# Performance work log

Measured on AMD Instinct MI355X. Metric: run time of the kernel, lower is better.

The kernel has to match this reference:

```python
import jax, jax.numpy as jnp
import numpy as np

N_RNA, N_DIS = 40000, 3000
E_EDGES, T = 600000, 10000
RNA_IN, D_FEAT, HID, EXP_D = 512, 256, 512, 256
N_EXP, HEADS = 8, 8
HD = HID // HEADS          # per-head dim inside HANConv
MHA_HD = EXP_D // HEADS    # per-head dim in cross-attention
FUSION = 2 * HID


def setup_inputs() -> dict:
    key = jax.random.key(0)
    ks = iter(jax.random.split(key, 48))
    def nrm(shape, s=0.02):
        return jax.random.normal(next(ks), shape, dtype=jnp.float32) * s
    inp = {
        "x_rna": jax.random.normal(next(ks), (N_RNA, RNA_IN), dtype=jnp.float32),
        "x_dis": jax.random.normal(next(ks), (N_DIS, D_FEAT), dtype=jnp.float32),
        "Wd": nrm((RNA_IN, D_FEAT)), "bd": jnp.zeros((RNA_IN,), jnp.float32),
        "Wp_r": nrm((HID, RNA_IN)), "bp_r": jnp.zeros((HID,), jnp.float32),
        "Wp_d": nrm((HID, RNA_IN)), "bp_d": jnp.zeros((HID,), jnp.float32),
        "a_src_rd": nrm((HEADS, HD), 0.1), "a_dst_rd": nrm((HEADS, HD), 0.1),
        "a_src_dr": nrm((HEADS, HD), 0.1), "a_dst_dr": nrm((HEADS, HD), 0.1),
        "kW": nrm((HID, HID)), "kb": jnp.zeros((HID,), jnp.float32),
        "qv": nrm((HID,), 0.1),
        "Wl": nrm((HID, HID)), "bl": jnp.zeros((HID,), jnp.float32),
        "W_exp": nrm((N_EXP, FUSION, EXP_D)), "b_exp": jnp.zeros((N_EXP, EXP_D), jnp.float32),
        "W_gate": nrm((4, HID, N_EXP)),
        "W_head": nrm((4, 2 * EXP_D, EXP_D)), "b_head": jnp.zeros((4, EXP_D), jnp.float32),
        "in_w": nrm((3 * EXP_D, EXP_D)), "in_b": jnp.zeros((3 * EXP_D,), jnp.float32),
        "out_w": nrm((EXP_D, EXP_D)), "out_b": jnp.zeros((EXP_D,), jnp.float32),
        "Wdp": nrm((EXP_D, HID)), "bdp": jnp.zeros((EXP_D,), jnp.float32),
        "ei_rd_src": jax.random.randint(next(ks), (E_EDGES,), 0, N_RNA),
        "ei_rd_dst": jax.random.randint(next(ks), (E_EDGES,), 0, N_DIS),
        "ei_dr_src": jax.random.randint(next(ks), (E_EDGES,), 0, N_DIS),
        "ei_dr_dst": jax.random.randint(next(ks), (E_EDGES,), 0, N_RNA),
        "idx_rels": jax.random.randint(next(ks), (4, T), 0, N_RNA),
    }
    return inp


def _han_edge(x_src, x_dst, ei_src, ei_dst, a_src, a_dst, n_dst):
    # x_*: [N, H, D]; GAT-style attention with softmax per destination node (PyG HANConv edge step)
    as_ = (x_src * a_src).sum(-1)                                 # [Ns, H]
    ad_ = (x_dst * a_dst).sum(-1)                                 # [Nd, H]
    alpha = jax.nn.leaky_relu(as_[ei_src] + ad_[ei_dst], 0.2)     # [E, H]
    amax = jax.ops.segment_max(alpha, ei_dst, num_segments=n_dst)
    ex = jnp.exp(alpha - amax[ei_dst])
    den = jax.ops.segment_sum(ex, ei_dst, num_segments=n_dst)
    w = ex / (den[ei_dst] + 1e-16)
    msg = x_src[ei_src] * w[:, :, None]                           # [E, H, D]
    out = jax.ops.segment_sum(msg, ei_dst, num_segments=n_dst)    # [Nd, H, D]
    return jax.nn.relu(out.reshape(n_dst, -1))


def _semantic(outs, kW, kb, qv):
    # outs: [M, N, F]; metapath-level (semantic) attention from HANConv
    s = (jnp.tanh(outs @ kW.T + kb).mean(axis=1) * qv).sum(-1)    # [M]
    beta = jax.nn.softmax(s)
    return (beta[:, None, None] * outs).sum(0)


def reference(x_rna, x_dis, Wd, bd, Wp_r, bp_r, Wp_d, bp_d,
              a_src_rd, a_dst_rd, a_src_dr, a_dst_dr,
              kW, kb, qv, Wl, bl, W_exp, b_exp, W_gate, W_head, b_head,
              in_w, in_b, out_w, out_b, Wdp, bdp,
              ei_rd_src, ei_rd_dst, ei_dr_src, ei_dr_dst, idx_rels):
    # ---- HAN encoder ----
    xd = x_dis @ Wd.T + bd                                        # disease feat -> rna_in_dim
    hr0 = (x_rna @ Wp_r.T + bp_r).reshape(N_RNA, HEADS, HD)
    hd0 = (xd @ Wp_d.T + bp_d).reshape(N_DIS, HEADS, HD)
    out_dis = _han_edge(hr0, hd0, ei_rd_src, ei_rd_dst, a_src_rd, a_dst_rd, N_DIS)
    out_rna = _han_edge(hd0, hr0, ei_dr_src, ei_dr_dst, a_src_dr, a_dst_dr, N_RNA)
    h_rna = _semantic(out_rna[None], kW, kb, qv) @ Wl.T + bl      # shared final lin
    h_dis = _semantic(out_dis[None], kW, kb, qv) @ Wl.T + bl
    # ---- MoE with per-relation gating ----
    d_global = h_dis.mean(axis=0)
    fusion = jnp.concatenate([h_rna, jnp.broadcast_to(d_global, h_rna.shape)], axis=1)  # [N, 2H]
    E = jax.nn.relu(jnp.einsum('nf,efd->ned', fusion, W_exp) + b_exp)  # [N, Nexp, Ed]
    h_t = h_rna[idx_rels]                                         # [4, T, H]
    scores = jnp.einsum('rth,rhe->rte', h_t, W_gate)              # raw gate scores (no softmax)
    u = (E[idx_rels] * scores[..., None]).sum(axis=2)             # [4, T, Ed]
    U = u.mean(axis=1)                                            # [4, Ed]
    # ---- cross attention over 4 task tokens ----
    qkv = U @ in_w.T + in_b
    q, k, v = jnp.split(qkv, 3, axis=-1)
    def heads(z):
        return z.reshape(4, HEADS, MHA_HD).transpose(1, 0, 2)     # [H, 4, dh]
    qh, kh, vh = heads(q), heads(k), heads(v)
    attn = jax.nn.softmax(jnp.einsum('htd,hsd->hts', qh, kh) / np.float32(np.sqrt(MHA_HD)), axis=-1)
    o = jnp.einsum('hts,hsd->htd', attn, vh).transpose(1, 0, 2).reshape(4, EXP_D)
    U_prime = o @ out_w.T + out_b                                 # [4, Ed]
    # ---- per-relation heads and disease scores ----
    cross = jnp.broadcast_to(U_prime[:, None, :], u.shape)
    cat = jnp.concatenate([u, cross], axis=-1)                    # [4, T, 2Ed]
    p = jax.nn.relu(jnp.einsum('rtc,rcd->rtd', cat, W_head) + b_head[:, None, :])
    d_proj = h_dis @ Wdp.T + bdp                                  # [Ndis, Ed]
    return jax.nn.sigmoid(jnp.einsum('rtd,md->rtm', p, d_proj))   # [4, T, Ndis]
```

## Files before the change

kernel.cpp:

```cpp
#include <hip/hip_runtime.h>
#include <math.h>

constexpr int NRNA = 40000;
constexpr int NDIS = 3000;
constexpr int NEDG = 600000;
constexpr int TREL = 10000;

typedef __attribute__((ext_vector_type(8))) short bh8;
typedef __attribute__((ext_vector_type(4))) float f32x4;

__device__ inline float bf2f(ushort x) {
    union { uint u; float f; } v; v.u = ((uint)x) << 16; return v.f;
}
__device__ inline ushort f2bf(float f) {
    union { float f; uint u; } v; v.f = f;
    uint u = v.u;
    uint r = (u + 0x7fffu + ((u >> 16) & 1u)) >> 16;
    return (ushort)r;
}
__device__ inline float bflo(uint w) { union { uint u; float f; } v; v.u = w << 16; return v.f; }
__device__ inline float bfhi(uint w) { union { uint u; float f; } v; v.u = w & 0xffff0000u; return v.f; }

__device__ inline void gload16(const ushort* g, ushort* l) {
    __builtin_amdgcn_global_load_lds(
        (const __attribute__((address_space(1))) unsigned int*)(const void*)g,
        (__attribute__((address_space(3))) unsigned int*)(void*)l, 16, 0, 0);
}

__global__ __launch_bounds__(256) void conv_bf16(const float* __restrict__ in,
                                                 ushort* __restrict__ out, long n)
{
    long g = ((long)blockIdx.x * 256 + threadIdx.x) * 4;
    if (g >= n) return;
    float4 v = *(const float4*)(in + g);
    ushort4 o;
    o.x = f2bf(v.x); o.y = f2bf(v.y); o.z = f2bf(v.z); o.w = f2bf(v.w);
    *(ushort4*)(out + g) = o;
}

__global__ __launch_bounds__(256) void transpose_wexp(const float* __restrict__ W,
                                                      ushort* __restrict__ out)
{
    long g = (long)blockIdx.x * 256 + threadIdx.x;
    int e = (int)(g >> 17), d = (int)((g >> 9) & 255), f = (int)(g & 511);
    out[g] = f2bf(W[(long)e * 262144 + (long)f * 256 + d]);
}

__global__ __launch_bounds__(256) void transpose_whead(const float* __restrict__ W,
                                                       ushort* __restrict__ out)
{
    long g = (long)blockIdx.x * 256 + threadIdx.x;
    int r = (int)(g >> 16), d = (int)((g >> 8) & 255), c = (int)(g & 255);
    out[g] = f2bf(W[(long)r * 131072 + (long)c * 256 + d]);
}

__global__ void transpose_wgate(const float* __restrict__ W, float* __restrict__ out)
{
    int g = blockIdx.x * 256 + threadIdx.x;
    int r = g >> 12, e = (g >> 9) & 7, k = g & 511;
    out[g] = W[(long)r * 4096 + (long)k * 8 + e];
}

template<int ACT>
__global__ __launch_bounds__(256) void gemm_mfma(
    const ushort* __restrict__ A, const ushort* __restrict__ B,
    const float* __restrict__ bias, float* __restrict__ Cf, ushort* __restrict__ Cb,
    const int* __restrict__ idx,
    int M, int N, int K, long sA, long sB, long sBias, long sC)
{
    __shared__ ushort smem[16384];
    ushort* As = smem;
    ushort* Bs = smem + 8192;
    const int bz = blockIdx.z;
    const ushort* Ab = A + (long)bz * sA;
    const ushort* Bb = B + (long)bz * sB;
    const float* biasb = bias ? (bias + (long)bz * sBias) : nullptr;
    const int row0 = blockIdx.y * 128, col0 = blockIdx.x * 128;

    const int tid = threadIdx.x, wid = tid >> 6, lane = tid & 63;
    const int wr = wid >> 1, wc = wid & 1;

    const int lrow = lane >> 3;
    const int lk = (((lane & 7) ^ lrow) * 8);
    const ushort* ap0[4]; const ushort* bp0[4];
    ushort* la[4]; ushort* lb[4];
#pragma unroll
    for (int i = 0; i < 4; ++i) {
        int c = wid * 4 + i;
        int ra = row0 + c * 8 + lrow; ra = ra < M ? ra : M - 1;
        int rs = idx ? idx[ra] : ra;
        ap0[i] = Ab + (long)rs * K + lk;
        int cb = col0 + c * 8 + lrow; cb = cb < N ? cb : N - 1;
        bp0[i] = Bb + (long)cb * K + lk;
        la[i] = As + c * 512;
        lb[i] = Bs + c * 512;
    }

    f32x4 acc[4][4];
#pragma unroll
    for (int i = 0; i < 4; ++i)
#pragma unroll
        for (int n = 0; n < 4; ++n) acc[i][n] = (f32x4){0.f, 0.f, 0.f, 0.f};

    const int fr = lane & 15, fq = lane >> 4;
    const int sw0 = (fq ^ (fr & 7)) * 8;
    const ushort* paRow = As + (wr * 64 + fr) * 64;
    const ushort* pbRow = Bs + (wc * 64 + fr) * 64;

    for (int k0 = 0; k0 < K; k0 += 64) {
#pragma unroll
// ... 37 lines not shown
            int cl = (tid & 15) * 4;
            int m = row0 + rl, col = col0 + H * 64 + cl;
            if (m < M && col < N) {
                f32x4 v = *(const f32x4*)(cs + rl * 64 + cl);
                if (biasb) {
                    float4 bv = *(const float4*)(biasb + col);
                    v[0] += bv.x; v[1] += bv.y; v[2] += bv.z; v[3] += bv.w;
                }
                if (ACT == 1) {
#pragma unroll
                    for (int q = 0; q < 4; ++q) v[q] = fmaxf(v[q], 0.f);
                } else if (ACT == 2) {
#pragma unroll
                    for (int q = 0; q < 4; ++q) v[q] = 1.f / (1.f + __expf(-v[q]));
                }
                long o = (long)bz * sC + (long)m * N + col;
                if (Cf) *(f32x4*)(Cf + o) = v;
                if (Cb) {
                    ushort4 ob;
                    ob.x = f2bf(v[0]); ob.y = f2bf(v[1]); ob.z = f2bf(v[2]); ob.w = f2bf(v[3]);
                    *(ushort4*)(Cb + o) = ob;
                }
            }
        }
        __syncthreads();
    }
}

__global__ __launch_bounds__(256) void moe_mfma(
    const ushort* __restrict__ h, const ushort* __restrict__ WexpT,
    const float* __restrict__ c_exp, const float* __restrict__ S,
    const int* __restrict__ idx, ushort* __restrict__ up)
{
    __shared__ ushort smem[16384];
    __shared__ float sS[128 * 8];
    __shared__ float sC[8 * 128];
    ushort* As = smem;
    ushort* Bs = smem + 8192;
    const int row0 = blockIdx.y * 128, col0 = blockIdx.x * 128;
    const int z = blockIdx.z, e0 = z * 4;
    const int tid = threadIdx.x, wid = tid >> 6, lane = tid & 63;
    const int wr = wid >> 1, wc = wid & 1;
    constexpr int M = 4 * TREL;

    for (int i = tid; i < 1024; i += 256) {
        int rr = i >> 3, e = i & 7;
        sS[i] = S[(long)(row0 + rr) * 8 + e];
        int ee = i >> 7, cc = i & 127;
        sC[i] = c_exp[ee * 256 + col0 + cc];
    }

    const int lrow = lane >> 3;
    const int lk = (((lane & 7) ^ lrow) * 8);
    const ushort* ap0[4]; const ushort* bp0[4];
    ushort* la[4]; ushort* lb[4];
#pragma unroll
    for (int i = 0; i < 4; ++i) {
        int c = wid * 4 + i;
        int ra = row0 + c * 8 + lrow;
        ap0[i] = h + (long)idx[ra] * 512 + lk;
        bp0[i] = WexpT + (long)(col0 + c * 8 + lrow) * 512 + (long)e0 * 131072 + lk;
        la[i] = As + c * 512;
        lb[i] = Bs + c * 512;
    }

    const int fr = lane & 15, fq = lane >> 4;
    const int sw0 = (fq ^ (fr & 7)) * 8;
    const ushort* paRow = As + (wr * 64 + fr) * 64;
    const ushort* pbRow = Bs + (wc * 64 + fr) * 64;

    f32x4 uacc[4][4];
#pragma unroll
    for (int i = 0; i < 4; ++i)
#pragma unroll
        for (int n = 0; n < 4; ++n) uacc[i][n] = (f32x4){0.f, 0.f, 0.f, 0.f};
    __syncthreads();

    for (int el = 0; el < 4; ++el) {
        const int e = e0 + el;
        f32x4 acc[4][4];
#pragma unroll
        for (int i = 0; i < 4; ++i)
#pragma unroll
            for (int n = 0; n < 4; ++n) acc[i][n] = (f32x4){0.f, 0.f, 0.f, 0.f};
        const long boff = (long)el * 131072;
        for (int k0 = 0; k0 < 512; k0 += 64) {
#pragma unroll
            for (int i = 0; i < 4; ++i) gload16(ap0[i] + k0, la[i]);
#pragma unroll
            for (int i = 0; i < 4; ++i) gload16(bp0[i] + boff + k0, lb[i]);
            __syncthreads();
#pragma unroll
            for (int kk = 0; kk < 2; ++kk) {
                const int sw = kk ? (sw0 ^ 32) : sw0;
                bh8 af[4], bf[4];
#pragma unroll
                for (int i = 0; i < 4; ++i) af[i] = *(const bh8*)(paRow + i * 1024 + sw);
#pragma unroll
                for (int n = 0; n < 4; ++n) bf[n] = *(const bh8*)(pbRow + n * 1024 + sw);
#pragma unroll
                for (int i = 0; i < 4; ++i)
#pragma unroll
                    for (int n = 0; n < 4; ++n)
                        acc[i][n] = __builtin_amdgcn_mfma_f32_16x16x32_bf16(af[i], bf[n], acc[i][n], 0, 0, 0);
            }
            __syncthreads();
        }
#pragma unroll
        for (int i = 0; i < 4; ++i) {
            int rl = wr * 64 + i * 16 + fq * 4;
#pragma unroll
            for (int n = 0; n < 4; ++n) {
                int cl = wc * 64 + n * 16 + fr;
                float c = sC[e * 128 + cl];
#pragma unroll
                for (int r = 0; r < 4; ++r) {
                    float s = sS[(rl + r) * 8 + e];
                    float v = acc[i][n][r] + c;
                    uacc[i][n][r] = fmaf(s, fmaxf(v, 0.f), uacc[i][n][r]);
                }
            }
        }
    }

    float* cs = (float*)smem;
    ushort* upz = up + (long)z * M * 256;
#pragma unroll
    for (int H = 0; H < 2; ++H) {
        if (wc == H) {
#pragma unroll
            for (int i = 0; i < 4; ++i)
#pragma unroll
                for (int n = 0; n < 4; ++n)
#pragma unroll
                    for (int r = 0; r < 4; ++r)
                        cs[(wr * 64 + i * 16 + fq * 4 + r) * 64 + n * 16 + fr] = uacc[i][n][r];
        }
        __syncthreads();
#pragma unroll
        for (int it = 0; it < 8; ++it) {
            int rl = it * 16 + (tid >> 4);
            int cl = (tid & 15) * 4;
            f32x4 v = *(const f32x4*)(cs + rl * 64 + cl);
            int m = row0 + rl, col = col0 + H * 64 + cl;
            ushort4 ob;
            ob.x = f2bf(v[0]); ob.y = f2bf(v[1]); ob.z = f2bf(v[2]); ob.w = f2bf(v[3]);
            *(ushort4*)(upz + (long)m * 256 + col) = ob;
        }
        __syncthreads();
    }
}

__global__ __launch_bounds__(256) void moe_combine(const ushort* __restrict__ up,
                                                   ushort* __restrict__ u)
{
    constexpr long TOT = (long)4 * TREL * 256;
    long g = ((long)blockIdx.x * 256 + threadIdx.x) * 4;
    if (g >= TOT) return;
    ushort4 a = *(const ushort4*)(up + g);
    ushort4 b = *(const ushort4*)(up + TOT + g);
    ushort4 o;
    o.x = f2bf(bf2f(a.x) + bf2f(b.x));
    o.y = f2bf(bf2f(a.y) + bf2f(b.y));
    o.z = f2bf(bf2f(a.z) + bf2f(b.z));
    o.w = f2bf(bf2f(a.w) + bf2f(b.w));
    *(ushort4*)(u + g) = o;
}

__global__ void dot_heads_bf(const ushort* __restrict__ x, const float* __restrict__ a,
                             float* __restrict__ out, int nodes)
{
    long g = (long)blockIdx.x * 256 + threadIdx.x;
    if (g >= (long)nodes * 8) return;
    int node = (int)(g >> 3), h = (int)(g & 7);
    const ushort* xp = x + (long)node * 512 + h * 64;
    const float* ap = a + h * 64;
    float s = 0.f;
#pragma unroll
    for (int d = 0; d < 64; d += 8) {
        uint4 xv = *(const uint4*)(xp + d);
        float4 a0 = *(const float4*)(ap + d);
        float4 a1 = *(const float4*)(ap + d + 4);
        s += bflo(xv.x) * a0.x + bfhi(xv.x) * a0.y + bflo(xv.y) * a0.z + bfhi(xv.y) * a0.w;
        s += bflo(xv.z) * a1.x + bfhi(xv.z) * a1.y + bflo(xv.w) * a1.z + bfhi(xv.w) * a1.w;
    }
    out[g] = s;
}

__global__ void hist_kernel(const int* __restrict__ dst, int* __restrict__ deg, int E)
{
    int g = blockIdx.x * 256 + threadIdx.x;
    if (g < E) atomicAdd(&deg[dst[g]], 1);
}

__global__ __launch_bounds__(1024) void scan_blocks(const int* __restrict__ in,
                                                    int* __restrict__ tmp,
                                                    int* __restrict__ bsum, int n)
{
    __shared__ int wsum[16];
    const int tid = threadIdx.x, lane = tid & 63, wid = tid >> 6;
    int base = blockIdx.x * 1024;
    int v = (base + tid < n) ? in[base + tid] : 0;
    int s = v;
#pragma unroll
    for (int off = 1; off < 64; off <<= 1) {
        int t = __shfl_up(s, off, 64);
        if (lane >= off) s += t;
    }
    if (lane == 63) wsum[wid] = s;
    __syncthreads();
    if (wid == 0) {
        int w = (lane < 16) ? wsum[lane] : 0;
#pragma unroll
        for (int off = 1; off < 16; off <<= 1) {
            int t = __shfl_up(w, off, 64);
            if (lane >= off) w += t;
        }
        if (lane < 16) wsum[lane] = w;
    }
// ... 12 lines not shown
        int t = __shfl_up(v, off, 64);
        if (lane >= off) v += t;
    }
    if (lane < nb) bsum[lane] = v;
}

__global__ __launch_bounds__(1024) void scan_finish(const int* __restrict__ in,
                                                    const int* __restrict__ tmp,
                                                    const int* __restrict__ bsum,
                                                    int* __restrict__ offs,
                                                    int* __restrict__ cur, int n, int nb)
{
    int base = blockIdx.x * 1024;
    int i = base + threadIdx.x;
    if (i < n) {
        int pre = (blockIdx.x == 0) ? 0 : bsum[blockIdx.x - 1];
        int v = tmp[i] - in[i] + pre;
        offs[i] = v;
        cur[i] = v;
    }
    if (i == 0) offs[n] = bsum[nb - 1];
}

__global__ void scatter_kernel(const int* __restrict__ src, const int* __restrict__ dst,
                               int* __restrict__ cur, int* __restrict__ csr_src, int E)
{
    int g = blockIdx.x * 256 + threadIdx.x;
    if (g < E) {
        int p = atomicAdd(&cur[dst[g]], 1);
        csr_src[p] = src[g];
    }
}

__global__ __launch_bounds__(256) void han_aggregate(
    const int* __restrict__ offs, const int* __restrict__ csr_src,
    const float* __restrict__ as_, const float* __restrict__ ad_,
    const ushort* __restrict__ x_src, ushort* __restrict__ out)
{
    const int node = blockIdx.x;
    const int tid = threadIdx.x;
    const int e0 = offs[node], e1 = offs[node + 1];
    const int ne = e1 - e0;

    __shared__ float s_amax[8], s_den[8];
    __shared__ float s_ex[32 * 8];
    __shared__ int   s_srcs[32];
    __shared__ float s_red[256];
    __shared__ float s_part[4 * 512];

    const int myh = tid & 7;
    const float my_ad = ad_[node * 8 + myh];

    float mx = -3.0e38f;
    for (int i = tid; i < ne * 8; i += 256) {
        int src = csr_src[e0 + (i >> 3)];
        float al = as_[(long)src * 8 + myh] + my_ad;
        al = al >= 0.f ? al : 0.2f * al;
        mx = fmaxf(mx, al);
    }
    s_red[tid] = mx;
    __syncthreads();
    if (tid < 8) {
        float m = -3.0e38f;
        for (int j = tid; j < 256; j += 8) m = fmaxf(m, s_red[j]);
        s_amax[tid] = m;
    }
    __syncthreads();
    const float myamax = s_amax[myh];

    const int g = tid >> 6, l64 = tid & 63, col8 = l64 * 8, gh = l64 >> 3;
    float acc[8];
#pragma unroll
    for (int k = 0; k < 8; ++k) acc[k] = 0.f;
    float dpart = 0.f;

    for (int c0 = 0; c0 < ne; c0 += 32) {
        const int nc = min(32, ne - c0);
        __syncthreads();
        if (tid < nc * 8) {
            int ec = tid >> 3;
            int src = csr_src[e0 + c0 + ec];
            if (myh == 0) s_srcs[ec] = src;
            float al = as_[(long)src * 8 + myh] + my_ad;
            al = al >= 0.f ? al : 0.2f * al;
            float ex = __expf(al - myamax);
            s_ex[ec * 8 + myh] = ex;
            dpart += ex;
        }
        __syncthreads();
        for (int j2 = 0; j2 < 8; ++j2) {
            int jj = j2 * 4 + g;
            if (jj >= nc) break;
            float w = s_ex[jj * 8 + gh];
            uint4 xv = *(const uint4*)(x_src + (long)s_srcs[jj] * 512 + col8);
            acc[0] = fmaf(w, bflo(xv.x), acc[0]);
            acc[1] = fmaf(w, bfhi(xv.x), acc[1]);
            acc[2] = fmaf(w, bflo(xv.y), acc[2]);
            acc[3] = fmaf(w, bfhi(xv.y), acc[3]);
            acc[4] = fmaf(w, bflo(xv.z), acc[4]);
            acc[5] = fmaf(w, bfhi(xv.z), acc[5]);
            acc[6] = fmaf(w, bflo(xv.w), acc[6]);
            acc[7] = fmaf(w, bfhi(xv.w), acc[7]);
        }
    }

    s_red[tid] = dpart;
    __syncthreads();
    if (tid < 8) {
        float s = 0.f;
        for (int j = tid; j < 256; j += 8) s += s_red[j];
        s_den[tid] = s;
    }
#pragma unroll
    for (int k = 0; k < 8; ++k) s_part[g * 512 + col8 + k] = acc[k];
    __syncthreads();

    int c2 = tid * 2;
    float v0 = s_part[c2] + s_part[512 + c2] + s_part[1024 + c2] + s_part[1536 + c2];
    float v1 = s_part[c2 + 1] + s_part[512 + c2 + 1] + s_part[1024 + c2 + 1] + s_part[1536 + c2 + 1];
    float den = s_den[c2 >> 6] + 1e-16f;
    ushort2 o;
    o.x = f2bf(fmaxf(v0 / den, 0.f));
    o.y = f2bf(fmaxf(v1 / den, 0.f));
    *(ushort2*)(out + (long)node * 512 + c2) = o;
}

__global__ __launch_bounds__(512) void hdis_colsum_partial(const float* __restrict__ h_dis,
                                                           float* __restrict__ part)
{
    int c = blockIdx.x, d = threadIdx.x;
    int r0 = c * 200;
    float s = 0.f;
    for (int r = r0; r < r0 + 200; ++r) s += h_dis[(long)r * 512 + d];
    part[c * 512 + d] = s;
}
__global__ __launch_bounds__(512) void hdis_colsum_finish(const float* __restrict__ part,
                                                          float* __restrict__ dg)
{
    int d = threadIdx.x;
    float s = 0.f;
    for (int c = 0; c < 15; ++c) s += part[c * 512 + d];
    dg[d] = s * (1.f / NDIS);
}

__global__ void cexp_kernel(const float* __restrict__ dg, const float* __restrict__ W_exp,
                            const float* __restrict__ b_exp, float* __restrict__ c_exp)
{
    int e = blockIdx.x, d = threadIdx.x;
    const float* W = W_exp + (long)e * 1024 * 256 + 512 * 256 + d;
    float s = b_exp[e * 256 + d];
    for (int f = 0; f < 512; ++f) s = fmaf(dg[f], W[(long)f * 256], s);
    c_exp[e * 256 + d] = s;
}

__global__ __launch_bounds__(256) void scores2(const ushort* __restrict__ h,
                                               const float* __restrict__ WgT,
                                               const int* __restrict__ idx,
                                               float* __restrict__ S)
{
    __shared__ float sW[8 * 512];
    const int r = blockIdx.y;
    const int tid = threadIdx.x;
    for (int i = tid; i < 4096; i += 256) sW[i] = WgT[(long)r * 4096 + i];
    __syncthreads();
    int n = blockIdx.x * 256 + tid;
    if (n >= TREL) return;
    int gi = r * TREL + n;
    const ushort* hp = h + (long)idx[gi] * 512;
    float acc[8];
#pragma unroll
    for (int e = 0; e < 8; ++e) acc[e] = 0.f;
    for (int k = 0; k < 512; k += 8) {
        uint4 hv = *(const uint4*)(hp + k);
        float hf[8];
        hf[0] = bflo(hv.x); hf[1] = bfhi(hv.x); hf[2] = bflo(hv.y); hf[3] = bfhi(hv.y);
        hf[4] = bflo(hv.z); hf[5] = bfhi(hv.z); hf[6] = bflo(hv.w); hf[7] = bfhi(hv.w);
#pragma unroll
        for (int e = 0; e < 8; ++e)
#pragma unroll
            for (int j = 0; j < 8; ++j)
                acc[e] = fmaf(hf[j], sW[e * 512 + k + j], acc[e]);
    }
#pragma unroll
    for (int e = 0; e < 8; ++e) S[(long)gi * 8 + e] = acc[e];
// ... 102 lines not shown
    const float* a_dst_dr = (const float*)d_in[11];
    const float* Wl       = (const float*)d_in[15];
    const float* bl       = (const float*)d_in[16];
    const float* W_exp    = (const float*)d_in[17];
    const float* b_exp    = (const float*)d_in[18];
    const float* W_gate   = (const float*)d_in[19];
    const float* W_head   = (const float*)d_in[20];
    const float* b_head   = (const float*)d_in[21];
    const float* in_w     = (const float*)d_in[22];
    const float* in_b     = (const float*)d_in[23];
    const float* out_w    = (const float*)d_in[24];
    const float* out_b    = (const float*)d_in[25];
    const float* Wdp      = (const float*)d_in[26];
    const float* bdp      = (const float*)d_in[27];
    const int* ei_rd_src  = (const int*)d_in[28];
    const int* ei_rd_dst  = (const int*)d_in[29];
    const int* ei_dr_src  = (const int*)d_in[30];
    const int* ei_dr_dst  = (const int*)d_in[31];
    const int* idx_rels   = (const int*)d_in[32];
    float* out = (float*)d_out;

    char* ws = (char*)d_ws;
    size_t off = 0;
    auto alloc = [&](size_t bytes) -> void* {
        off = (off + 255) & ~(size_t)255;
        void* p = ws + off;
        off += bytes;
        return p;
    };
    ushort* xrb      = (ushort*)alloc((size_t)NRNA * 512 * 2);
    ushort* hr0b     = (ushort*)alloc((size_t)NRNA * 512 * 2);
    ushort* u_bf     = (ushort*)alloc((size_t)4 * TREL * 256 * 2);
    ushort* p_bf     = (ushort*)alloc((size_t)4 * TREL * 256 * 2);
    ushort* up_bf    = (ushort*)alloc((size_t)2 * 4 * TREL * 256 * 2);
    ushort* xdb      = (ushort*)alloc((size_t)NDIS * 256 * 2);
    ushort* xd_bf    = (ushort*)alloc((size_t)NDIS * 512 * 2);
    ushort* hd0b     = (ushort*)alloc((size_t)NDIS * 512 * 2);
    ushort* outdis_b = (ushort*)alloc((size_t)NDIS * 512 * 2);
    ushort* hdis_b   = (ushort*)alloc((size_t)NDIS * 512 * 2);
    ushort* dproj_b  = (ushort*)alloc((size_t)NDIS * 256 * 2);
    float*  hdis_f   = (float*)alloc((size_t)NDIS * 512 * 4);
    ushort* Wdb    = (ushort*)alloc((size_t)512 * 256 * 2);
    ushort* Wprb   = (ushort*)alloc((size_t)512 * 512 * 2);
    ushort* Wpdb   = (ushort*)alloc((size_t)512 * 512 * 2);
    ushort* Wlb    = (ushort*)alloc((size_t)512 * 512 * 2);
    ushort* Wdpb   = (ushort*)alloc((size_t)256 * 512 * 2);
    ushort* WexpT  = (ushort*)alloc((size_t)8 * 256 * 512 * 2);
    ushort* WheadT = (ushort*)alloc((size_t)4 * 256 * 256 * 2);
    float*  WgT    = (float*)alloc((size_t)4 * 8 * 512 * 4);
    float* as_rd   = (float*)alloc((size_t)NRNA * 8 * 4);
    float* ad_rd   = (float*)alloc((size_t)NDIS * 8 * 4);
    float* as_dr   = (float*)alloc((size_t)NDIS * 8 * 4);
    float* ad_dr   = (float*)alloc((size_t)NRNA * 8 * 4);
    float* S       = (float*)alloc((size_t)4 * TREL * 8 * 4);
    float* dg_part = (float*)alloc((size_t)15 * 512 * 4);
    float* dg      = (float*)alloc((size_t)512 * 4);
    float* c_exp   = (float*)alloc((size_t)8 * 256 * 4);
    float* u_part  = (float*)alloc((size_t)4 * 32 * 256 * 4);
    float* U       = (float*)alloc((size_t)4 * 256 * 4);
    float* Up      = (float*)alloc((size_t)4 * 256 * 4);
    float* c_head  = (float*)alloc((size_t)4 * 256 * 4);
    int* deg_rd  = (int*)alloc((size_t)NDIS * 4);
    int* offs_rd = (int*)alloc((size_t)(NDIS + 1) * 4);
    int* cur_rd  = (int*)alloc((size_t)NDIS * 4);
    int* csr_rd  = (int*)alloc((size_t)NEDG * 4);
    int* deg_dr  = (int*)alloc((size_t)NRNA * 4);
    int* offs_dr = (int*)alloc((size_t)(NRNA + 1) * 4);
    int* cur_dr  = (int*)alloc((size_t)NRNA * 4);
    int* csr_dr  = (int*)alloc((size_t)NEDG * 4);
    int* scan_tmp = (int*)alloc((size_t)NRNA * 4);
    int* scan_bs  = (int*)alloc((size_t)64 * 4);
    if (off > ws_size) return;

    ushort* outrna_b = xrb;
    ushort* hrna_b   = hr0b;

    const dim3 blk(256);

    conv_bf16<<<dim3(20000), blk, 0, stream>>>(x_rna, xrb, (long)NRNA * 512);
    conv_bf16<<<dim3(750),   blk, 0, stream>>>(x_dis, xdb, (long)NDIS * 256);
    conv_bf16<<<dim3(128),   blk, 0, stream>>>(Wd,   Wdb,  512 * 256);
    conv_bf16<<<dim3(256),   blk, 0, stream>>>(Wp_r, Wprb, 512 * 512);
    conv_bf16<<<dim3(256),   blk, 0, stream>>>(Wp_d, Wpdb, 512 * 512);
    conv_bf16<<<dim3(256),   blk, 0, stream>>>(Wl,   Wlb,  512 * 512);
    conv_bf16<<<dim3(128),   blk, 0, stream>>>(Wdp,  Wdpb, 256 * 512);
    transpose_wexp<<<dim3(4096), blk, 0, stream>>>(W_exp, WexpT);
    transpose_whead<<<dim3(1024), blk, 0, stream>>>(W_head, WheadT);
    transpose_wgate<<<dim3(64), blk, 0, stream>>>(W_gate, WgT);

    gemm_mfma<0><<<dim3(4, 24), blk, 0, stream>>>(
        xdb, Wdb, bd, nullptr, xd_bf, nullptr, NDIS, 512, 256, 0, 0, 0, 0);
    gemm_mfma<0><<<dim3(4, 313), blk, 0, stream>>>(
        xrb, Wprb, bp_r, nullptr, hr0b, nullptr, NRNA, 512, 512, 0, 0, 0, 0);
    gemm_mfma<0><<<dim3(4, 24), blk, 0, stream>>>(
        xd_bf, Wpdb, bp_d, nullptr, hd0b, nullptr, NDIS, 512, 512, 0, 0, 0, 0);

    dot_heads_bf<<<dim3((NRNA * 8) / 256), blk, 0, stream>>>(hr0b, a_src_rd, as_rd, NRNA);
    dot_heads_bf<<<dim3((NDIS * 8 + 255) / 256), blk, 0, stream>>>(hd0b, a_dst_rd, ad_rd, NDIS);
    dot_heads_bf<<<dim3((NDIS * 8 + 255) / 256), blk, 0, stream>>>(hd0b, a_src_dr, as_dr, NDIS);
    dot_heads_bf<<<dim3((NRNA * 8) / 256), blk, 0, stream>>>(hr0b, a_dst_dr, ad_dr, NRNA);

    hipMemsetAsync(deg_rd, 0, NDIS * 4, stream);
    hipMemsetAsync(deg_dr, 0, NRNA * 4, stream);
    hist_kernel<<<dim3((NEDG + 255) / 256), blk, 0, stream>>>(ei_rd_dst, deg_rd, NEDG);
    hist_kernel<<<dim3((NEDG + 255) / 256), blk, 0, stream>>>(ei_dr_dst, deg_dr, NEDG);
    scan_blocks<<<dim3(3), dim3(1024), 0, stream>>>(deg_rd, scan_tmp, scan_bs, NDIS);
    scan_bsums<<<dim3(1), dim3(64), 0, stream>>>(scan_bs, 3);
    scan_finish<<<dim3(3), dim3(1024), 0, stream>>>(deg_rd, scan_tmp, scan_bs, offs_rd, cur_rd, NDIS, 3);
    scan_blocks<<<dim3(40), dim3(1024), 0, stream>>>(deg_dr, scan_tmp, scan_bs, NRNA);
    scan_bsums<<<dim3(1), dim3(64), 0, stream>>>(scan_bs, 40);
    scan_finish<<<dim3(40), dim3(1024), 0, stream>>>(deg_dr, scan_tmp, scan_bs, offs_dr, cur_dr, NRNA, 40);
    scatter_kernel<<<dim3((NEDG + 255) / 256), blk, 0, stream>>>(ei_rd_src, ei_rd_dst, cur_rd, csr_rd, NEDG);
    scatter_kernel<<<dim3((NEDG + 255) / 256), blk, 0, stream>>>(ei_dr_src, ei_dr_dst, cur_dr, csr_dr, NEDG);

    han_aggregate<<<dim3(NDIS), blk, 0, stream>>>(offs_rd, csr_rd, as_rd, ad_rd, hr0b, outdis_b);
    han_aggregate<<<dim3(NRNA), blk, 0, stream>>>(offs_dr, csr_dr, as_dr, ad_dr, hd0b, outrna_b);

    gemm_mfma<0><<<dim3(4, 313), blk, 0, stream>>>(
        outrna_b, Wlb, bl, nullptr, hrna_b, nullptr, NRNA, 512, 512, 0, 0, 0, 0);
    gemm_mfma<0><<<dim3(4, 24), blk, 0, stream>>>(
        outdis_b, Wlb, bl, hdis_f, hdis_b, nullptr, NDIS, 512, 512, 0, 0, 0, 0);

    hdis_colsum_partial<<<dim3(15), dim3(512), 0, stream>>>(hdis_f, dg_part);
    hdis_colsum_finish<<<dim3(1), dim3(512), 0, stream>>>(dg_part, dg);
    cexp_kernel<<<dim3(8), blk, 0, stream>>>(dg, W_exp, b_exp, c_exp);
    scores2<<<dim3(40, 4), blk, 0, stream>>>(hrna_b, WgT, idx_rels, S);

    moe_mfma<<<dim3(2, 320, 2), blk, 0, stream>>>(hrna_b, WexpT, c_exp, S, idx_rels, up_bf);
    moe_combine<<<dim3(10240), blk, 0, stream>>>(up_bf, u_bf);

    u_mean_partial<<<dim3(32, 4), blk, 0, stream>>>(u_bf, u_part);
    u_mean_finish<<<dim3(4), blk, 0, stream>>>(u_part, U);
    cross_attn_kernel<<<dim3(1), blk, 0, stream>>>(U, in_w, in_b, out_w, out_b, Up);
    chead_kernel<<<dim3(4), blk, 0, stream>>>(Up, W_head, b_head, c_head);

    gemm_mfma<1><<<dim3(2, 79, 4), blk, 0, stream>>>(
        u_bf, WheadT, c_head, nullptr, p_bf, nullptr, TREL, 256, 256,
        (long)TREL * 256, 65536, 256, (long)TREL * 256);

    gemm_mfma<0><<<dim3(2, 24), blk, 0, stream>>>(
        hdis_b, Wdpb, bdp, nullptr, dproj_b, nullptr, NDIS, 256, 512, 0, 0, 0, 0);

    gemm_mfma<2><<<dim3(24, 320), blk, 0, stream>>>(
        p_bf, dproj_b, nullptr, out, nullptr, nullptr, 4 * TREL, NDIS, 256, 0, 0, 0, 0);
}
```

Before: 1.398 ms.

## Restructure MoE, HAN aggregation, and add XCD-aware block swizzle to GEMMs

Adds an XCD-aware block index remap to the large GEMMs and the MoE kernel so neighbouring tiles share an L2. MoE now computes two experts per block, sharing the A tile, over four z-slices, and the combine kernel sums four partials. HAN aggregation switches from one block per node to one wavefront per node with shuffle reductions, which removes block-wide syncs. It also fuses the per-head dot kernels pairwise and splits the c_exp reduction across more blocks. The cost is a larger partial buffer and more combine traffic.

Result: faster. 1.294 ms (-7.4%).

```diff
diff --git a/kernel.cpp b/kernel.cpp
--- a/kernel.cpp
+++ b/kernel.cpp
@@ -25,6 +25,11 @@
     __builtin_amdgcn_global_load_lds(
         (const __attribute__((address_space(1))) unsigned int*)(const void*)g,
         (__attribute__((address_space(3))) unsigned int*)(void*)l, 16, 0, 0);
+}
+
+__device__ inline int xcd_swz(int f, int n) {
+    int q = n >> 3, r = n & 7, xcd = f & 7, i = f >> 3;
+    return (xcd < r) ? (xcd * (q + 1) + i) : (r * (q + 1) + (xcd - r) * q + i);
 }
 
 __global__ __launch_bounds__(256) void conv_bf16(const float* __restrict__ in,
@@ -61,7 +66,7 @@
     out[g] = W[(long)r * 4096 + (long)k * 8 + e];
 }
 
-template<int ACT>
+template<int ACT, bool SWZ>
 __global__ __launch_bounds__(256) void gemm_mfma(
     const ushort* __restrict__ A, const ushort* __restrict__ B,
     const float* __restrict__ bias, float* __restrict__ Cf, ushort* __restrict__ Cb,
@@ -71,11 +76,17 @@
     __shared__ ushort smem[16384];
     ushort* As = smem;
     ushort* Bs = smem + 8192;
+    int bx = blockIdx.x, by = blockIdx.y;
+    if (SWZ) {
+        int n = gridDim.x * gridDim.y;
+        int s = xcd_swz(by * gridDim.x + bx, n);
+        bx = s % gridDim.x; by = s / gridDim.x;
+    }
     const int bz = blockIdx.z;
     const ushort* Ab = A + (long)bz * sA;
     const ushort* Bb = B + (long)bz * sB;
     const float* biasb = bias ? (bias + (long)bz * sBias) : nullptr;
-    const int row0 = blockIdx.y * 128, col0 = blockIdx.x * 128;
+    const int row0 = by * 128, col0 = bx * 128;
 
     const int tid = threadIdx.x, wid = tid >> 6, lane = tid & 63;
     const int wr = wid >> 1, wc = wid & 1;
@@ -179,93 +190,106 @@
     const float* __restrict__ c_exp, const float* __restrict__ S,
     const int* __restrict__ idx, ushort* __restrict__ up)
 {
-    __shared__ ushort smem[16384];
-    __shared__ float sS[128 * 8];
-    __shared__ float sC[8 * 128];
-    ushort* As = smem;
-    ushort* Bs = smem + 8192;
-    const int row0 = blockIdx.y * 128, col0 = blockIdx.x * 128;
-    const int z = blockIdx.z, e0 = z * 4;
+    __shared__ ushort smem[24576];
+    __shared__ float sS[128 * 2];
+    __shared__ float sC[2 * 128];
+    ushort* As  = smem;
+    ushort* Bs0 = smem + 8192;
+    ushort* Bs1 = smem + 16384;
+    int bx = blockIdx.x, by = blockIdx.y;
+    {
+        int n = gridDim.x * gridDim.y;
+        int s = xcd_swz(by * gridDim.x + bx, n);
+        bx = s % gridDim.x; by = s / gridDim.x;
+    }
+    const int row0 = by * 128, col0 = bx * 128;
+    const int z = blockIdx.z, e0 = z * 2;
     const int tid = threadIdx.x, wid = tid >> 6, lane = tid & 63;
     const int wr = wid >> 1, wc = wid & 1;
     constexpr int M = 4 * TREL;
 
-    for (int i = tid; i < 1024; i += 256) {
-        int rr = i >> 3, e = i & 7;
-        sS[i] = S[(long)(row0 + rr) * 8 + e];
-        int ee = i >> 7, cc = i & 127;
-        sC[i] = c_exp[ee * 256 + col0 + cc];
+    if (tid < 256) {
+        int rr = tid >> 1, e = tid & 1;
+        sS[tid] = S[(long)(row0 + rr) * 8 + e0 + e];
+    }
+    if (tid < 256) {
+        int e = tid >> 7, cc = tid & 127;
+        sC[tid] = c_exp[(e0 + e) * 256 + col0 + cc];
     }
 
     const int lrow = lane >> 3;
     const int lk = (((lane & 7) ^ lrow) * 8);
     const ushort* ap0[4]; const ushort* bp0[4];
-    ushort* la[4]; ushort* lb[4];
+    ushort* la[4]; ushort* lb0[4]; ushort* lb1[4];
 #pragma unroll
     for (int i = 0; i < 4; ++i) {
         int c = wid * 4 + i;
         int ra = row0 + c * 8 + lrow;
         ap0[i] = h + (long)idx[ra] * 512 + lk;
         bp0[i] = WexpT + (long)(col0 + c * 8 + lrow) * 512 + (long)e0 * 131072 + lk;
-        la[i] = As + c * 512;
-        lb[i] = Bs + c * 512;
+        la[i]  = As  + c * 512;
+        lb0[i] = Bs0 + c * 512;
+        lb1[i] = Bs1 + c * 512;
     }
 
     const int fr = lane & 15, fq = lane >> 4;
     const int sw0 = (fq ^ (fr & 7)) * 8;
-    const ushort* paRow = As + (wr * 64 + fr) * 64;
-    const ushort* pbRow = Bs + (wc * 64 + fr) * 64;
-
-    f32x4 uacc[4][4];
+    const ushort* paRow  = As  + (wr * 64 + fr) * 64;
+    const ushort* pb0Row = Bs0 + (wc * 64 + fr) * 64;
+    const ushort* pb1Row = Bs1 + (wc * 64 + fr) * 64;
+
+    f32x4 acc0[4][4], acc1[4][4];
 #pragma unroll
     for (int i = 0; i < 4; ++i)
 #pragma unroll
-        for (int n = 0; n < 4; ++n) uacc[i][n] = (f32x4){0.f, 0.f, 0.f, 0.f};
+        for (int n = 0; n < 4; ++n) {
+            acc0[i][n] = (f32x4){0.f, 0.f, 0.f, 0.f};
+            acc1[i][n] = (f32x4){0.f, 0.f, 0.f, 0.f};
+        }
     __syncthreads();
 
-    for (int el = 0; el < 4; ++el) {
-        const int e = e0 + el;
-        f32x4 acc[4][4];
-#pragma unroll
-        for (int i = 0; i < 4; ++i)
-#pragma unroll
-            for (int n = 0; n < 4; ++n) acc[i][n] = (f32x4){0.f, 0.f, 0.f, 0.f};
-        const long boff = (long)el * 131072;
-        for (int k0 = 0; k0 < 512; k0 += 64) {
-#pragma unroll
-            for (int i = 0; i < 4; ++i) gload16(ap0[i] + k0, la[i]);
-#pragma unroll
-            for (int i = 0; i < 4; ++i) gload16(bp0[i] + boff + k0, lb[i]);
-            __syncthreads();
-#pragma unroll
-            for (int kk = 0; kk < 2; ++kk) {
-                const int sw = kk ? (sw0 ^ 32) : sw0;
-                bh8 af[4], bf[4];
-#pragma unroll
-                for (int i = 0; i < 4; ++i) af[i] = *(const bh8*)(paRow + i * 1024 + sw);
-#pragma unroll
-                for (int n = 0; n < 4; ++n) bf[n] = *(const bh8*)(pbRow + n * 1024 + sw);
-#pragma unroll
-                for (int i = 0; i < 4; ++i)
-#pragma unroll
-                    for (int n = 0; n < 4; ++n)
-                        acc[i][n] = __builtin_amdgcn_mfma_f32_16x16x32_bf16(af[i], bf[n], acc[i][n], 0, 0, 0);
-            }
-            __syncthreads();
-        }
-#pragma unroll
-        for (int i = 0; i < 4; ++i) {
-            int rl = wr * 64 + i * 16 + fq * 4;
-#pragma unroll
-            for (int n = 0; n < 4; ++n) {
-                int cl = wc * 64 + n * 16 + fr;
-                float c = sC[e * 128 + cl];
-#pragma unroll
-                for (int r = 0; r < 4; ++r) {
-                    float s = sS[(rl + r) * 8 + e];
-                    float v = acc[i][n][r] + c;
-                    uacc[i][n][r] = fmaf(s, fmaxf(v, 0.f), uacc[i][n][r]);
+    for (int k0 = 0; k0 < 512; k0 += 64) {
+#pragma unroll
+        for (int i = 0; i < 4; ++i) gload16(ap0[i] + k0, la[i]);
+#pragma unroll
+        for (int i = 0; i < 4; ++i) gload16(bp0[i] + k0, lb0[i]);
+#pragma unroll
+        for (int i = 0; i < 4; ++i) gload16(bp0[i] + 131072 + k0, lb1[i]);
+        __syncthreads();
+#pragma unroll
+        for (int kk = 0; kk < 2; ++kk) {
+            const int sw = kk ? (sw0 ^ 32) : sw0;
+            bh8 af[4], b0[4], b1[4];
+#pragma unroll
+            for (int i = 0; i < 4; ++i) af[i] = *(const bh8*)(paRow + i * 1024 + sw);
+#pragma unroll
+            for (int n = 0; n < 4; ++n) b0[n] = *(const bh8*)(pb0Row + n * 1024 + sw);
+#pragma unroll
+            for (int n = 0; n < 4; ++n) b1[n] = *(const bh8*)(pb1Row + n * 1024 + sw);
+#pragma unroll
+            for (int i = 0; i < 4; ++i)
+#pragma unroll
+                for (int n = 0; n < 4; ++n) {
+                    acc0[i][n] = __builtin_amdgcn_mfma_f32_16x16x32_bf16(af[i], b0[n], acc0[i][n], 0, 0, 0);
+                    acc1[i][n] = __builtin_amdgcn_mfma_f32_16x16x32_bf16(af[i], b1[n], acc1[i][n], 0, 0, 0);
                 }
+        }
+        __syncthreads();
+    }
+
+#pragma unroll
+    for (int i = 0; i < 4; ++i) {
+        int rl = wr * 64 + i * 16 + fq * 4;
+#pragma unroll
+        for (int n = 0; n < 4; ++n) {
+            int cl = wc * 64 + n * 16 + fr;
+            float c0 = sC[cl], c1 = sC[128 + cl];
+#pragma unroll
+            for (int r = 0; r < 4; ++r) {
+                float s0 = sS[(rl + r) * 2 + 0];
+                float s1 = sS[(rl + r) * 2 + 1];
+                acc0[i][n][r] = s0 * fmaxf(acc0[i][n][r] + c0, 0.f)
+                              + s1 * fmaxf(acc1[i][n][r] + c1, 0.f);
             }
         }
     }
@@ -281,7 +305,7 @@
                 for (int n = 0; n < 4; ++n)
 #pragma unroll
                     for (int r = 0; r < 4; ++r)
-                        cs[(wr * 64 + i * 16 + fq * 4 + r) * 64 + n * 16 + fr] = uacc[i][n][r];
+                        cs[(wr * 64 + i * 16 + fq * 4 + r) * 64 + n * 16 + fr] = acc0[i][n][r];
         }
         __syncthreads();
 #pragma unroll
@@ -304,34 +328,40 @@
     constexpr long TOT = (long)4 * TREL * 256;
     long g = ((long)blockIdx.x * 256 + threadIdx.x) * 4;
     if (g >= TOT) return;
-    ushort4 a = *(const ushort4*)(up + g);
-    ushort4 b = *(const ushort4*)(up + TOT + g);
+    float a[4] = {0.f, 0.f, 0.f, 0.f};
+#pragma unroll
+    for (int z = 0; z < 4; ++z) {
+        ushort4 v = *(const ushort4*)(up + z * TOT + g);
+        a[0] += bf2f(v.x); a[1] += bf2f(v.y); a[2] += bf2f(v.z); a[3] += bf2f(v.w);
+    }
     ushort4 o;
-    o.x = f2bf(bf2f(a.x) + bf2f(b.x));
-    o.y = f2bf(bf2f(a.y) + bf2f(b.y));
-    o.z = f2bf(bf2f(a.z) + bf2f(b.z));
-    o.w = f2bf(bf2f(a.w) + bf2f(b.w));
+    o.x = f2bf(a[0]); o.y = f2bf(a[1]); o.z = f2bf(a[2]); o.w = f2bf(a[3]);
     *(ushort4*)(u + g) = o;
 }
 
-__global__ void dot_heads_bf(const ushort* __restrict__ x, const float* __restrict__ a,
-                             float* __restrict__ out, int nodes)
+__global__ void dot_heads2(const ushort* __restrict__ x,
+                           const float* __restrict__ a1, const float* __restrict__ a2,
+                           float* __restrict__ o1, float* __restrict__ o2, int nodes)
 {
     long g = (long)blockIdx.x * 256 + threadIdx.x;
     if (g >= (long)nodes * 8) return;
     int node = (int)(g >> 3), h = (int)(g & 7);
     const ushort* xp = x + (long)node * 512 + h * 64;
-    const float* ap = a + h * 64;
-    float s = 0.f;
+    const float* p1 = a1 + h * 64;
+    const float* p2 = a2 + h * 64;
+    float s1 = 0.f, s2 = 0.f;
 #pragma unroll
     for (int d = 0; d < 64; d += 8) {
         uint4 xv = *(const uint4*)(xp + d);
-        float4 a0 = *(const float4*)(ap + d);
-        float4 a1 = *(const float4*)(ap + d + 4);
-        s += bflo(xv.x) * a0.x + bfhi(xv.x) * a0.y + bflo(xv.y) * a0.z + bfhi(xv.y) * a0.w;
-        s += bflo(xv.z) * a1.x + bfhi(xv.z) * a1.y + bflo(xv.w) * a1.z + bfhi(xv.w) * a1.w;
-    }
-    out[g] = s;
+        float xf[8] = { bflo(xv.x), bfhi(xv.x), bflo(xv.y), bfhi(xv.y),
+                        bflo(xv.z), bfhi(xv.z), bflo(xv.w), bfhi(xv.w) };
+#pragma unroll
+        for (int j = 0; j < 8; ++j) {
+            s1 = fmaf(xf[j], p1[d + j], s1);
+            s2 = fmaf(xf[j], p2[d + j], s2);
+        }
+    }
+    o1[g] = s1; o2[g] = s2;
 }
 
 __global__ void hist_kernel(const int* __restrict__ dst, int* __restrict__ deg, int E)
@@ -410,97 +440,78 @@
     }
 }
 
-__global__ __launch_bounds__(256) void han_aggregate(
+__global__ __launch_bounds__(256) void han_wave(
     const int* __restrict__ offs, const int* __restrict__ csr_src,
     const float* __restrict__ as_, const float* __restrict__ ad_,
-    const ushort* __restrict__ x_src, ushort* __restrict__ out)
-{
-    const int node = blockIdx.x;
-    const int tid = threadIdx.x;
-    const int e0 = offs[node], e1 = offs[node + 1];
-    const int ne = e1 - e0;
-
-    __shared__ float s_amax[8], s_den[8];
-    __shared__ float s_ex[32 * 8];
-    __shared__ int   s_srcs[32];
-    __shared__ float s_red[256];
-    __shared__ float s_part[4 * 512];
-
-    const int myh = tid & 7;
+    const ushort* __restrict__ x_src, ushort* __restrict__ out, int nnode)
+{
+    __shared__ float s_ex[4][64];
+    __shared__ int   s_src[4][8];
+    __shared__ float s_den[4][8];
+    const int w = threadIdx.x >> 6, lane = threadIdx.x & 63;
+    const int node = blockIdx.x * 4 + w;
+    if (node >= nnode) return;
+    const int e0 = offs[node], ne = offs[node + 1] - e0;
+    const int myh = lane & 7, grp = lane >> 3;
     const float my_ad = ad_[node * 8 + myh];
 
     float mx = -3.0e38f;
-    for (int i = tid; i < ne * 8; i += 256) {
-        int src = csr_src[e0 + (i >> 3)];
+    for (int t = grp; t < ne; t += 8) {
+        int src = csr_src[e0 + t];
         float al = as_[(long)src * 8 + myh] + my_ad;
         al = al >= 0.f ? al : 0.2f * al;
         mx = fmaxf(mx, al);
     }
-    s_red[tid] = mx;
-    __syncthreads();
-    if (tid < 8) {
-        float m = -3.0e38f;
-        for (int j = tid; j < 256; j += 8) m = fmaxf(m, s_red[j]);
-        s_amax[tid] = m;
-    }
-    __syncthreads();
-    const float myamax = s_amax[myh];
-
-    const int g = tid >> 6, l64 = tid & 63, col8 = l64 * 8, gh = l64 >> 3;
+#pragma unroll
+    for (int m = 8; m < 64; m <<= 1) mx = fmaxf(mx, __shfl_xor(mx, m, 64));
+
+    float den = 0.f;
     float acc[8];
 #pragma unroll
     for (int k = 0; k < 8; ++k) acc[k] = 0.f;
-    float dpart = 0.f;
-
-    for (int c0 = 0; c0 < ne; c0 += 32) {
-        const int nc = min(32, ne - c0);
-        __syncthreads();
-        if (tid < nc * 8) {
-            int ec = tid >> 3;
-            int src = csr_src[e0 + c0 + ec];
-            if (myh == 0) s_srcs[ec] = src;
+    const int colbase = lane * 8;
+
+    for (int c0 = 0; c0 < ne; c0 += 8) {
+        const int nc = min(8, ne - c0);
+        float ex = 0.f;
+        int src = 0;
+        if (grp < nc) {
+            src = csr_src[e0 + c0 + grp];
             float al = as_[(long)src * 8 + myh] + my_ad;
             al = al >= 0.f ? al : 0.2f * al;
-            float ex = __expf(al - myamax);
-            s_ex[ec * 8 + myh] = ex;
-            dpart += ex;
-        }
-        __syncthreads();
-        for (int j2 = 0; j2 < 8; ++j2) {
-            int jj = j2 * 4 + g;
-            if (jj >= nc) break;
-            float w = s_ex[jj * 8 + gh];
-            uint4 xv = *(const uint4*)(x_src + (long)s_srcs[jj] * 512 + col8);
-            acc[0] = fmaf(w, bflo(xv.x), acc[0]);
-            acc[1] = fmaf(w, bfhi(xv.x), acc[1]);
-            acc[2] = fmaf(w, bflo(xv.y), acc[2]);
-            acc[3] = fmaf(w, bfhi(xv.y), acc[3]);
-            acc[4] = fmaf(w, bflo(xv.z), acc[4]);
-            acc[5] = fmaf(w, bfhi(xv.z), acc[5]);
-            acc[6] = fmaf(w, bflo(xv.w), acc[6]);
-            acc[7] = fmaf(w, bfhi(xv.w), acc[7]);
-        }
-    }
-
-    s_red[tid] = dpart;
-    __syncthreads();
-    if (tid < 8) {
-        float s = 0.f;
-        for (int j = tid; j < 256; j += 8) s += s_red[j];
-        s_den[tid] = s;
-    }
-#pragma unroll
-    for (int k = 0; k < 8; ++k) s_part[g * 512 + col8 + k] = acc[k];
-    __syncthreads();
-
-    int c2 = tid * 2;
-    float v0 = s_part[c2] + s_part[512 + c2] + s_part[1024 + c2] + s_part[1536 + c2];
-    float v1 = s_part[c2 + 1] + s_part[512 + c2 + 1] + s_part[1024 + c2 + 1] + s_part[1536 + c2 + 1];
-    float den = s_den[c2 >> 6] + 1e-16f;
-    ushort2 o;
-    o.x = f2bf(fmaxf(v0 / den, 0.f));
-    o.y = f2bf(fmaxf(v1 / den, 0.f));
-    *(ushort2*)(out + (long)node * 512 + c2) = o;
+            ex = __expf(al - mx);
+            den += ex;
+        }
+        s_ex[w][grp * 8 + myh] = ex;
+        if (myh == 0) s_src[w][grp] = src;
+        asm volatile("s_waitcnt lgkmcnt(0)" ::: "memory");
+        for (int j = 0; j < nc; ++j) {
+            float wg = s_ex[w][j * 8 + grp];
+            uint4 xv = *(const uint4*)(x_src + (long)s_src[w][j] * 512 + colbase);
+            acc[0] = fmaf(wg, bflo(xv.x), acc[0]);
+            acc[1] = fmaf(wg, bfhi(xv.x), acc[1]);
+            acc[2] = fmaf(wg, bflo(xv.y), acc[2]);
+            acc[3] = fmaf(wg, bfhi(xv.y), acc[3]);
+            acc[4] = fmaf(wg, bflo(xv.z), acc[4]);
+            acc[5] = fmaf(wg, bfhi(xv.z), acc[5]);
+            acc[6] = fmaf(wg, bflo(xv.w), acc[6]);
+            acc[7] = fmaf(wg, bfhi(xv.w), acc[7]);
+        }
+        __builtin_amdgcn_wave_barrier();
+    }
+
+#pragma unroll
+    for (int m = 8; m < 64; m <<= 1) den += __shfl_xor(den, m, 64);
+    if (grp == 0) s_den[w][myh] = den;
+    asm volatile("s_waitcnt lgkmcnt(0)" ::: "memory");
+    float d = s_den[w][grp] + 1e-16f;
+
+    uint4 ov;
+    ov.x = (uint)f2bf(fmaxf(acc[0] / d, 0.f)) | ((uint)f2bf(fmaxf(acc[1] / d, 0.f)) << 16);
+    ov.y = (uint)f2bf(fmaxf(acc[2] / d, 0.f)) | ((uint)f2bf(fmaxf(acc[3] / d, 0.f)) << 16);
+    ov.z = (uint)f2bf(fmaxf(acc[4] / d, 0.f)) | ((uint)f2bf(fmaxf(acc[5] / d, 0.f)) << 16);
+    ov.w = (uint)f2bf(fmaxf(acc[6] / d, 0.f)) | ((uint)f2bf(fmaxf(acc[7] / d, 0.f)) << 16);
+    *(uint4*)(out + (long)node * 512 + colbase) = ov;
 }
 
 __global__ __launch_bounds__(512) void hdis_colsum_partial(const float* __restrict__ h_dis,
@@ -521,13 +532,22 @@
     dg[d] = s * (1.f / NDIS);
 }
 
-__global__ void cexp_kernel(const float* __restrict__ dg, const float* __restrict__ W_exp,
-                            const float* __restrict__ b_exp, float* __restrict__ c_exp)
+__global__ void cexp_part(const float* __restrict__ dg, const float* __restrict__ W_exp,
+                          float* __restrict__ part)
+{
+    int b = blockIdx.x;
+    int e = b >> 3, ch = b & 7, d = threadIdx.x;
+    const float* W = W_exp + (long)e * 262144 + (long)(512 + ch * 64) * 256 + d;
+    float s = 0.f;
+    for (int f = 0; f < 64; ++f) s = fmaf(dg[ch * 64 + f], W[(long)f * 256], s);
+    part[b * 256 + d] = s;
+}
+__global__ void cexp_fin(const float* __restrict__ part, const float* __restrict__ b_exp,
+                         float* __restrict__ c_exp)
 {
     int e = blockIdx.x, d = threadIdx.x;
-    const float* W = W_exp + (long)e * 1024 * 256 + 512 * 256 + d;
     float s = b_exp[e * 256 + d];
-    for (int f = 0; f < 512; ++f) s = fmaf(dg[f], W[(long)f * 256], s);
+    for (int ch = 0; ch < 8; ++ch) s += part[(e * 8 + ch) * 256 + d];
     c_exp[e * 256 + d] = s;
 }
 
@@ -696,7 +716,7 @@
     ushort* hr0b     = (ushort*)alloc((size_t)NRNA * 512 * 2);
     ushort* u_bf     = (ushort*)alloc((size_t)4 * TREL * 256 * 2);
     ushort* p_bf     = (ushort*)alloc((size_t)4 * TREL * 256 * 2);
-    ushort* up_bf    = (ushort*)alloc((size_t)2 * 4 * TREL * 256 * 2);
+    ushort* up_bf    = (ushort*)alloc((size_t)4 * 4 * TREL * 256 * 2);
     ushort* xdb      = (ushort*)alloc((size_t)NDIS * 256 * 2);
     ushort* xd_bf    = (ushort*)alloc((size_t)NDIS * 512 * 2);
     ushort* hd0b     = (ushort*)alloc((size_t)NDIS * 512 * 2);
@@ -720,6 +740,7 @@
     float* dg_part = (float*)alloc((size_t)15 * 512 * 4);
     float* dg      = (float*)alloc((size_t)512 * 4);
     float* c_exp   = (float*)alloc((size_t)8 * 256 * 4);
+    float* ce_part = (float*)alloc((size_t)64 * 256 * 4);
     float* u_part  = (float*)alloc((size_t)4 * 32 * 256 * 4);
     float* U       = (float*)alloc((size_t)4 * 256 * 4);
     float* Up      = (float*)alloc((size_t)4 * 256 * 4);
@@ -752,17 +773,15 @@
     transpose_whead<<<dim3(1024), blk, 0, stream>>>(W_head, WheadT);
     transpose_wgate<<<dim3(64), blk, 0, stream>>>(W_gate, WgT);
 
-    gemm_mfma<0><<<dim3(4, 24), blk, 0, stream>>>(
+    gemm_mfma<0,false><<<dim3(4, 24), blk, 0, stream>>>(
         xdb, Wdb, bd, nullptr, xd_bf, nullptr, NDIS, 512, 256, 0, 0, 0, 0);
-    gemm_mfma<0><<<dim3(4, 313), blk, 0, stream>>>(
+    gemm_mfma<0,true><<<dim3(4, 313), blk, 0, stream>>>(
         xrb, Wprb, bp_r, nullptr, hr0b, nullptr, NRNA, 512, 512, 0, 0, 0, 0);
-    gemm_mfma<0><<<dim3(4, 24), blk, 0, stream>>>(
+    gemm_mfma<0,false><<<dim3(4, 24), blk, 0, stream>>>(
         xd_bf, Wpdb, bp_d, nullptr, hd0b, nullptr, NDIS, 512, 512, 0, 0, 0, 0);
 
-    dot_heads_bf<<<dim3((NRNA * 8) / 256), blk, 0, stream>>>(hr0b, a_src_rd, as_rd, NRNA);
-    dot_heads_bf<<<dim3((NDIS * 8 + 255) / 256), blk, 0, stream>>>(hd0b, a_dst_rd, ad_rd, NDIS);
-    dot_heads_bf<<<dim3((NDIS * 8 + 255) / 256), blk, 0, stream>>>(hd0b, a_src_dr, as_dr, NDIS);
-    dot_heads_bf<<<dim3((NRNA * 8) / 256), blk, 0, stream>>>(hr0b, a_dst_dr, ad_dr, NRNA);
+    dot_heads2<<<dim3((NRNA * 8) / 256), blk, 0, stream>>>(hr0b, a_src_rd, a_dst_dr, as_rd, ad_dr, NRNA);
+    dot_heads2<<<dim3((NDIS * 8 + 255) / 256), blk, 0, stream>>>(hd0b, a_dst_rd, a_src_dr, ad_rd, as_dr, NDIS);
 
     hipMemsetAsync(deg_rd, 0, NDIS * 4, stream);
     hipMemsetAsync(deg_dr, 0, NRNA * 4, stream);
@@ -777,20 +796,21 @@
     scatter_kernel<<<dim3((NEDG + 255) / 256), blk, 0, stream>>>(ei_rd_src, ei_rd_dst, cur_rd, csr_rd, NEDG);
     scatter_kernel<<<dim3((NEDG + 255) / 256), blk, 0, stream>>>(ei_dr_src, ei_dr_dst, cur_dr, csr_dr, NEDG);
 
-    han_aggregate<<<dim3(NDIS), blk, 0, stream>>>(offs_rd, csr_rd, as_rd, ad_rd, hr0b, outdis_b);
-    han_aggregate<<<dim3(NRNA), blk, 0, stream>>>(offs_dr, csr_dr, as_dr, ad_dr, hd0b, outrna_b);
-
-    gemm_mfma<0><<<dim3(4, 313), blk, 0, stream>>>(
+    han_wave<<<dim3((NDIS + 3) / 4), blk, 0, stream>>>(offs_rd, csr_rd, as_rd, ad_rd, hr0b, outdis_b, NDIS);
+    han_wave<<<dim3(NRNA / 4), blk, 0, stream>>>(offs_dr, csr_dr, as_dr, ad_dr, hd0b, outrna_b, NRNA);
+
+    gemm_mfma<0,true><<<dim3(4, 313), blk, 0, stream>>>(
         outrna_b, Wlb, bl, nullptr, hrna_b, nullptr, NRNA, 512, 512, 0, 0, 0, 0);
-    gemm_mfma<0><<<dim3(4, 24), blk, 0, stream>>>(
+    gemm_mfma<0,false><<<dim3(4, 24), blk, 0, stream>>>(
         outdis_b, Wlb, bl, hdis_f, hdis_b, nullptr, NDIS, 512, 512, 0, 0, 0, 0);
 
     hdis_colsum_partial<<<dim3(15), dim3(512), 0, stream>>>(hdis_f, dg_part);
     hdis_colsum_finish<<<dim3(1), dim3(512), 0, stream>>>(dg_part, dg);
-    cexp_kernel<<<dim3(8), blk, 0, stream>>>(dg, W_exp, b_exp, c_exp);
+    cexp_part<<<dim3(64), blk, 0, stream>>>(dg, W_exp, ce_part);
+    cexp_fin<<<dim3(8), blk, 0, stream>>>(ce_part, b_exp, c_exp);
     scores2<<<dim3(40, 4), blk, 0, stream>>>(hrna_b, WgT, idx_rels, S);
 
-    moe_mfma<<<dim3(2, 320, 2), blk, 0, stream>>>(hrna_b, WexpT, c_exp, S, idx_rels, up_bf);
+    moe_mfma<<<dim3(2, 320, 4), blk, 0, stream>>>(hrna_b, WexpT, c_exp, S, idx_rels, up_bf);
     moe_combine<<<dim3(10240), blk, 0, stream>>>(up_bf, u_bf);
 
     u_mean_partial<<<dim3(32, 4), blk, 0, stream>>>(u_bf, u_part);
@@ -798,13 +818,13 @@
     cross_attn_kernel<<<dim3(1), blk, 0, stream>>>(U, in_w, in_b, out_w, out_b, Up);
     chead_kernel<<<dim3(4), blk, 0, stream>>>(Up, W_head, b_head, c_head);
 
-    gemm_mfma<1><<<dim3(2, 79, 4), blk, 0, stream>>>(
+    gemm_mfma<1,false><<<dim3(2, 79, 4), blk, 0, stream>>>(
         u_bf, WheadT, c_head, nullptr, p_bf, nullptr, TREL, 256, 256,
         (long)TREL * 256, 65536, 256, (long)TREL * 256);
 
-    gemm_mfma<0><<<dim3(2, 24), blk, 0, stream>>>(
+    gemm_mfma<0,false><<<dim3(2, 24), blk, 0, stream>>>(
         hdis_b, Wdpb, bdp, nullptr, dproj_b, nullptr, NDIS, 256, 512, 0, 0, 0, 0);
 
-    gemm_mfma<2><<<dim3(24, 320), blk, 0, stream>>>(
+    gemm_mfma<2,true><<<dim3(24, 320), blk, 0, stream>>>(
         p_bf, dproj_b, nullptr, out, nullptr, nullptr, 4 * TREL, NDIS, 256, 0, 0, 0, 0);
 }
```
